# Optimization experiments

Measured on AMD Instinct MI355X. Metric: run time of the kernel, lower is better.

## Reference

```python
import jax, jax.numpy as jnp
import numpy as np

D_MODEL, D_STATE, D_CONV = 1024, 16, 4
BATCH, SEQ = 4, 2048
LN_EPS = 1e-5


def setup_inputs() -> dict:
    key = jax.random.key(0)
    ks = jax.random.split(key, 16)
    s_in = 1.0 / np.sqrt(D_MODEL)
    inp = {
        "x": jax.random.normal(ks[0], (BATCH, SEQ, D_MODEL), dtype=jnp.float32),
        "W_in": jax.random.normal(ks[1], (D_MODEL, 2 * D_MODEL), dtype=jnp.float32) * s_in,
        "b_in": jnp.zeros((2 * D_MODEL,), jnp.float32),
        "conv_w": jax.random.normal(ks[2], (D_MODEL, 1, D_CONV), dtype=jnp.float32) * 0.5,
        "conv_b": jnp.zeros((D_MODEL,), jnp.float32),
        "W_bc": jax.random.normal(ks[3], (D_MODEL, 2 * D_STATE), dtype=jnp.float32) * s_in,
        "b_bc": jnp.zeros((2 * D_STATE,), jnp.float32),
        "W_dt": jax.random.normal(ks[4], (D_MODEL, D_MODEL), dtype=jnp.float32) * s_in,
        "b_dt": jnp.zeros((D_MODEL,), jnp.float32),
        "A_log": jax.random.normal(ks[5], (D_MODEL, D_STATE), dtype=jnp.float32),
        "D": jnp.ones((D_MODEL,), jnp.float32),
        "W_out": jax.random.normal(ks[6], (D_MODEL, D_MODEL), dtype=jnp.float32) * s_in,
        "b_out": jnp.zeros((D_MODEL,), jnp.float32),
        "ln_g": jnp.ones((D_MODEL,), jnp.float32),
        "ln_b": jnp.zeros((D_MODEL,), jnp.float32),
    }
    return inp


def _causal_depthwise_conv(x_btd, conv_w, conv_b):
    # x_btd: (B, T, D). torch Conv1d(groups=D, padding=d_conv-1)[:, :, :T] == causal left-pad conv
    x_bdt = jnp.transpose(x_btd, (0, 2, 1))  # NCH
    y = jax.lax.conv_general_dilated(
        x_bdt, conv_w,
        window_strides=(1,), padding=[(D_CONV - 1, 0)],
        dimension_numbers=("NCH", "OIH", "NCH"),
        feature_group_count=D_MODEL)
    y = y + conv_b[None, :, None]
    return jnp.transpose(y, (0, 2, 1))


def _mamba_forward(x, W_in, b_in, conv_w, conv_b, W_bc, b_bc, W_dt, b_dt,
                   A_log, D, W_out, b_out, ln_g, ln_b):
    B_, T, _ = x.shape
    proj = x @ W_in + b_in                       # (B, T, 2D)
    x_ssm, x_gate = jnp.split(proj, 2, axis=-1)
    x_conv = jax.nn.silu(_causal_depthwise_conv(x_ssm, conv_w, conv_b))  # (B,T,D)
    BC = x_conv @ W_bc + b_bc                    # (B,T,2N)
    Bm, Cm = jnp.split(BC, 2, axis=-1)           # each (B,T,N)
    dt = jax.nn.softplus(x_conv @ W_dt + b_dt)   # (B,T,D)
    A = -jnp.exp(A_log)                          # (D,N)

    def step(h, inp):
        xt, dtt, Bt, Ct = inp                    # (B,D),(B,D),(B,N),(B,N)
        dA = jnp.exp(dtt[:, :, None] * A)        # (B,D,N)
        h = h * dA + (dtt * xt)[:, :, None] * Bt[:, None, :]
        y = jnp.einsum('bdn,bn->bd', h, Ct) + xt * D
        return h, y

    h0 = jnp.zeros((B_, D_MODEL, D_STATE), x.dtype)
    xs = (jnp.swapaxes(x_conv, 0, 1), jnp.swapaxes(dt, 0, 1),
          jnp.swapaxes(Bm, 0, 1), jnp.swapaxes(Cm, 0, 1))
    _, ys = jax.lax.scan(step, h0, xs)           # (T,B,D)
    y = jnp.swapaxes(ys, 0, 1)

    y = y * jax.nn.silu(x_gate)
    out = y @ W_out + b_out
    res = out + x
    mu = jnp.mean(res, axis=-1, keepdims=True)
    var = jnp.var(res, axis=-1, keepdims=True)
    return (res - mu) * jax.lax.rsqrt(var + LN_EPS) * ln_g + ln_b


def reference(x, W_in, b_in, conv_w, conv_b, W_bc, b_bc, W_dt, b_dt,
              A_log, D, W_out, b_out, ln_g, ln_b):
    return _mamba_forward(x, W_in, b_in, conv_w, conv_b, W_bc, b_bc,
                          W_dt, b_dt, A_log, D, W_out, b_out, ln_g, ln_b)
```

## Files before the change

kernel.cpp:

```cpp
#include <hip/hip_runtime.h>
#include <stdint.h>

#define D_MODEL 1024
#define T_SEQ   2048
#define N_BATCH 4
#define M_ROWS  (N_BATCH*T_SEQ)
#define N_STATE 16
#define SEGS    32
#define SEGLEN  (T_SEQ/SEGS)
#define CHUNK   8
#define NCHUNK  (SEGLEN/CHUNK)

typedef float  f32x4  __attribute__((ext_vector_type(4)));
typedef __bf16 bf16x8 __attribute__((ext_vector_type(8)));
typedef __bf16 bf16x4 __attribute__((ext_vector_type(4)));

__device__ __forceinline__ void gload16(const void* g, void* l) {
  __builtin_amdgcn_global_load_lds(
      (const __attribute__((address_space(1))) uint32_t*)g,
      (__attribute__((address_space(3))) uint32_t*)l, 16, 0, 0);
}

__device__ __forceinline__ float sigmoidf_(float v){ return 1.f/(1.f+__expf(-v)); }

__global__ __launch_bounds__(256) void cast_bf16_kernel(const float* __restrict__ in,
                                                        __bf16* __restrict__ out, int n4){
  int i = blockIdx.x*256 + threadIdx.x;
  if (i >= n4) return;
  float4 v = ((const float4*)in)[i];
  bf16x4 o; o[0]=(__bf16)v.x; o[1]=(__bf16)v.y; o[2]=(__bf16)v.z; o[3]=(__bf16)v.w;
  ((bf16x4*)out)[i] = o;
}

__global__ __launch_bounds__(256) void transpose_cast_kernel(const float* __restrict__ W,
                                                             __bf16* __restrict__ out,
                                                             int K, int N){
  __shared__ float tile[32][33];
  const int tx = threadIdx.x, ty = threadIdx.y;
  const int n0 = blockIdx.x*32, k0 = blockIdx.y*32;
  #pragma unroll
  for (int i=0;i<4;i++)
    tile[ty+i*8][tx] = W[(size_t)(k0+ty+i*8)*N + n0+tx];
  __syncthreads();
  #pragma unroll
  for (int i=0;i<4;i++)
    out[(size_t)(n0+ty+i*8)*K + k0+tx] = (__bf16)tile[tx][ty+i*8];
}

#define BK 32

template<int EPI, int BM, int BN, int NT>
__global__ __launch_bounds__(NT)
void gemm_bt(const __bf16* __restrict__ A, const __bf16* __restrict__ Bt,
             int N, int K,
             const float* __restrict__ bias0, const float* __restrict__ bias1,
             float* __restrict__ out0, float* __restrict__ out1,
             const float* __restrict__ addx,
             __bf16* __restrict__ out0b, __bf16* __restrict__ out1b)
{
  constexpr int NWAVE = NT/64;
  constexpr int WC_N  = NWAVE/2;
  constexpr int WM    = BM/2;
  constexpr int WN    = BN/WC_N;
  constexpr int MR    = WM/16, NR = WN/16;

  __shared__ __align__(16) __bf16 As[2][BM*BK];
  __shared__ __align__(16) __bf16 Bs[2][BN*BK];
  const int tid = threadIdx.x, wave = tid>>6, lane = tid&63;

  const int orig = blockIdx.y * gridDim.x + blockIdx.x;
  const int nwg  = gridDim.x * gridDim.y;
  const int cpx  = nwg >> 3;
  const int swz  = (orig & 7) * cpx + (orig >> 3);
  const int m0 = (swz / gridDim.x) * BM;
  const int n0 = (swz % gridDim.x) * BN;
  const int wr = wave / WC_N, wc = wave % WC_N;

  f32x4 acc[MR][NR];
  #pragma unroll
  for (int a=0;a<MR;a++)
    #pragma unroll
    for (int b=0;b<NR;b++) acc[a][b] = (f32x4){0.f,0.f,0.f,0.f};

  const int c0 = tid, c1 = tid + NT;
  const int r0 = c0>>2, s0 = (c0&3)*8;
  const int r1 = c1>>2, s1 = (c1&3)*8;
  const int arow = wr*WM + (lane&15), brow = wc*WN + (lane&15);
  const int kg = (lane>>4)*8;

  gload16(&A [(size_t)(m0+r0)*K + s0], &As[0][c0*8]);
  gload16(&A [(size_t)(m0+r1)*K + s1], &As[0][c1*8]);
  gload16(&Bt[(size_t)(n0+r0)*K + s0], &Bs[0][c0*8]);
  gload16(&Bt[(size_t)(n0+r1)*K + s1], &Bs[0][c1*8]);
  __syncthreads();

  const int nIter = K/BK;
  int buf = 0;
  for (int it=0; it<nIter; ++it){
    if (it+1 < nIter){
      const int kn = (it+1)*BK;
      gload16(&A [(size_t)(m0+r0)*K + kn + s0], &As[buf^1][c0*8]);
      gload16(&A [(size_t)(m0+r1)*K + kn + s1], &As[buf^1][c1*8]);
      gload16(&Bt[(size_t)(n0+r0)*K + kn + s0], &Bs[buf^1][c0*8]);
      gload16(&Bt[(size_t)(n0+r1)*K + kn + s1], &Bs[buf^1][c1*8]);
    }
    bf16x8 af[MR], bfv[NR];
    #pragma unroll
    for (int m=0;m<MR;m++) af[m]  = *(const bf16x8*)&As[buf][(arow+m*16)*BK + kg];
    #pragma unroll
    for (int n=0;n<NR;n++) bfv[n] = *(const bf16x8*)&Bs[buf][(brow+n*16)*BK + kg];
    #pragma unroll
    for (int m=0;m<MR;m++)
      #pragma unroll
      for (int n=0;n<NR;n++)
        acc[m][n] = __builtin_amdgcn_mfma_f32_16x16x32_bf16(af[m], bfv[n], acc[m][n], 0,0,0);
    __syncthreads();
    buf ^= 1;
  }

  const int cr = (lane>>4)*4, cc = lane&15;
  #pragma unroll
  for (int m=0;m<MR;m++){
    const int row = m0 + wr*WM + m*16 + cr;
    #pragma unroll
    for (int n=0;n<NR;n++){
      const int col = n0 + wc*WN + n*16 + cc;
      if (col >= N) continue;
      #pragma unroll
      for (int r=0;r<4;r++){
        float v = acc[m][n][r];
        const size_t ri = (size_t)(row + r);
        if constexpr (EPI==0){
          v += bias0[col];
          if (col < D_MODEL) out0b[ri*D_MODEL + col] = (__bf16)v;
          else               out1b[ri*D_MODEL + (col-D_MODEL)] = (__bf16)(v * sigmoidf_(v));
        } else if constexpr (EPI==1){
          if (col < D_MODEL){
            v += bias0[col];
            const float sp = (v > 20.f) ? v : __logf(1.f + __expf(v));
            out0b[ri*D_MODEL + col] = (__bf16)sp;
          } else {
            v += bias1[col-D_MODEL];
            out1[ri*32 + (col-D_MODEL)] = v;
          }
        } else {
          v += bias0[col] + addx[ri*D_MODEL + col];
          out0[ri*D_MODEL + col] = v;
        }
      }
    }
  }
}

__global__ __launch_bounds__(256) void conv_silu_kernel(
    const __bf16* __restrict__ xssm, const float* __restrict__ cw, const float* __restrict__ cb,
    __bf16* __restrict__ xcb)
{
  const int bt = blockIdx.x;
  const int t  = bt & (T_SEQ-1);
  const int d  = threadIdx.x*4;
  float4 w[4];
  #pragma unroll
  for (int j=0;j<4;j++) w[j] = *(const float4*)&cw[(d+j)*4];
  float4 acc = *(const float4*)&cb[d];
  #pragma unroll
  for (int k=0;k<4;k++){
    const int tt = t-3+k;
    if (tt >= 0){
      bf16x4 xv = ((const bf16x4*)xssm)[((size_t)(bt-3+k)*D_MODEL + d)>>2];
      acc.x = fmaf((float)xv[0], ((const float*)&w[0])[k], acc.x);
      acc.y = fmaf((float)xv[1], ((const float*)&w[1])[k], acc.y);
      acc.z = fmaf((float)xv[2], ((const float*)&w[2])[k], acc.z);
      acc.w = fmaf((float)xv[3], ((const float*)&w[3])[k], acc.w);
    }
  }
  acc.x *= sigmoidf_(acc.x); acc.y *= sigmoidf_(acc.y);
  acc.z *= sigmoidf_(acc.z); acc.w *= sigmoidf_(acc.w);
  bf16x4 o; o[0]=(__bf16)acc.x; o[1]=(__bf16)acc.y; o[2]=(__bf16)acc.z; o[3]=(__bf16)acc.w;
  ((bf16x4*)xcb)[((size_t)bt*D_MODEL + d)>>2] = o;
}

__global__ __launch_bounds__(128) void scan_p1(
    const __bf16* __restrict__ xcb, const __bf16* __restrict__ dtb, const float* __restrict__ BCb,
    const float* __restrict__ A_log, float* __restrict__ Ebuf, float* __restrict__ Pbuf)
{
  const int tid = threadIdx.x;
  const int d = blockIdx.x*128 + tid;
  const int b = blockIdx.y, sg = blockIdx.z;
  float an[16];
  {
    f32x4 a0 = *(const f32x4*)&A_log[(size_t)d*16];
    f32x4 a1 = *(const f32x4*)&A_log[(size_t)d*16+4];
    f32x4 a2 = *(const f32x4*)&A_log[(size_t)d*16+8];
    f32x4 a3 = *(const f32x4*)&A_log[(size_t)d*16+12];
    #pragma unroll
    for (int n=0;n<4;n++){ an[n]=-__expf(a0[n]); an[4+n]=-__expf(a1[n]);
                           an[8+n]=-__expf(a2[n]); an[12+n]=-__expf(a3[n]); }
  }
  __shared__ float sB[2][CHUNK][16];
  const size_t base = (size_t)b*T_SEQ + (size_t)sg*SEGLEN;
  const int sr = tid>>4, sc = tid&15;

  float dtr[CHUNK], xcr[CHUNK];
  sB[0][sr][sc] = BCb[(base + sr)*32 + sc];
  #pragma unroll
  for (int t=0;t<CHUNK;t++){
    dtr[t] = (float)dtb[(base+t)*D_MODEL + d];
    xcr[t] = (float)xcb[(base+t)*D_MODEL + d];
  }
  __syncthreads();

  float h[16];
  #pragma unroll
  for (int n=0;n<16;n++) h[n]=0.f;
  float sdt = 0.f;

  for (int c=0;c<NCHUNK;c++){
    float dtn[CHUNK], xcn[CHUNK], bnv = 0.f;
    if (c+1 < NCHUNK){
      const size_t nb = base + (size_t)(c+1)*CHUNK;
      #pragma unroll
      for (int t=0;t<CHUNK;t++){
        dtn[t] = (float)dtb[(nb+t)*D_MODEL + d];
        xcn[t] = (float)xcb[(nb+t)*D_MODEL + d];
      }
      bnv = BCb[(nb + sr)*32 + sc];
    }
    const int cb = c&1;
    #pragma unroll
    for (int t=0;t<CHUNK;t++){
      const float dtv = dtr[t], u = dtv*xcr[t];
      sdt += dtv;
      #pragma unroll
      for (int n=0;n<16;n++){
        const float dA = __expf(dtv*an[n]);
        h[n] = fmaf(h[n], dA, u*sB[cb][t][n]);
      }
    }
    if (c+1 < NCHUNK){
      sB[cb^1][sr][sc] = bnv;
      #pragma unroll
      for (int t=0;t<CHUNK;t++){ dtr[t]=dtn[t]; xcr[t]=xcn[t]; }
    }
    __syncthreads();
  }
  const size_t o = ((((size_t)sg*N_BATCH)+b)*D_MODEL + d)*16;
  #pragma unroll
  for (int n=0;n<16;n++){
    Ebuf[o+n] = h[n];
    Pbuf[o+n] = __expf(an[n]*sdt);
  }
}

__global__ __launch_bounds__(256) void scan_p2(float* __restrict__ Ebuf,
                                               const float* __restrict__ Pbuf)
{
  const size_t g = (size_t)blockIdx.x*256 + threadIdx.x;
  float c = 0.f;
  #pragma unroll
  for (int s=0;s<SEGS;s++){
    const size_t idx = (size_t)s*(N_BATCH*D_MODEL*N_STATE) + g;
    const float e = Ebuf[idx];
    const float p = Pbuf[idx];
    Ebuf[idx] = c;
    c = fmaf(p, c, e);
  }
}

__global__ __launch_bounds__(128) void scan_p3(
    const __bf16* __restrict__ xcb, const __bf16* __restrict__ dtb, const float* __restrict__ BCb,
    const float* __restrict__ A_log, const float* __restrict__ Dvec,
    const __bf16* __restrict__ gsil, const float* __restrict__ Ebuf,
    __bf16* __restrict__ ybf)
{
  const int tid = threadIdx.x;
  const int d = blockIdx.x*128 + tid;
  const int b = blockIdx.y, sg = blockIdx.z;
  float an[16];
  {
    f32x4 a0 = *(const f32x4*)&A_log[(size_t)d*16];
    f32x4 a1 = *(const f32x4*)&A_log[(size_t)d*16+4];
    f32x4 a2 = *(const f32x4*)&A_log[(size_t)d*16+8];
    f32x4 a3 = *(const f32x4*)&A_log[(size_t)d*16+12];
    #pragma unroll
    for (int n=0;n<4;n++){ an[n]=-__expf(a0[n]); an[4+n]=-__expf(a1[n]);
                           an[8+n]=-__expf(a2[n]); an[12+n]=-__expf(a3[n]); }
  }
  const float Dd = Dvec[d];
  __shared__ float sBC[2][CHUNK][32];
  const size_t base = (size_t)b*T_SEQ + (size_t)sg*SEGLEN;
  const int sr = tid>>4, sc = tid&15;

  float h[16];
  {
    const size_t o = ((((size_t)sg*N_BATCH)+b)*D_MODEL + d)*16;
    f32x4 e0 = *(const f32x4*)&Ebuf[o];
    f32x4 e1 = *(const f32x4*)&Ebuf[o+4];
    f32x4 e2 = *(const f32x4*)&Ebuf[o+8];
    f32x4 e3 = *(const f32x4*)&Ebuf[o+12];
    #pragma unroll
    for (int n=0;n<4;n++){ h[n]=e0[n]; h[4+n]=e1[n]; h[8+n]=e2[n]; h[12+n]=e3[n]; }
  }

  float dtr[CHUNK], xcr[CHUNK], gsr[CHUNK];
  sBC[0][sr][sc]    = BCb[(base + sr)*32 + sc];
  sBC[0][sr][16+sc] = BCb[(base + sr)*32 + 16 + sc];
  #pragma unroll
  for (int t=0;t<CHUNK;t++){
    dtr[t] = (float)dtb[(base+t)*D_MODEL + d];
    xcr[t] = (float)xcb[(base+t)*D_MODEL + d];
    gsr[t] = (float)gsil[(base+t)*D_MODEL + d];
  }
  __syncthreads();

  for (int c=0;c<NCHUNK;c++){
    float dtn[CHUNK], xcn[CHUNK], gsn[CHUNK], bnv=0.f, cnv=0.f;
    if (c+1 < NCHUNK){
      const size_t nb = base + (size_t)(c+1)*CHUNK;
      #pragma unroll
      for (int t=0;t<CHUNK;t++){
        dtn[t] = (float)dtb[(nb+t)*D_MODEL + d];
        xcn[t] = (float)xcb[(nb+t)*D_MODEL + d];
        gsn[t] = (float)gsil[(nb+t)*D_MODEL + d];
      }
      bnv = BCb[(nb + sr)*32 + sc];
      cnv = BCb[(nb + sr)*32 + 16 + sc];
    }
    const int cb = c&1;
    #pragma unroll
    for (int t=0;t<CHUNK;t++){
      const float dtv = dtr[t], xcv = xcr[t], u = dtv*xcv;
      #pragma unroll
      for (int n=0;n<16;n++){
        const float dA = __expf(dtv*an[n]);
        h[n] = fmaf(h[n], dA, u*sBC[cb][t][n]);
      }
      float yv = Dd*xcv;
      #pragma unroll
      for (int n=0;n<16;n++) yv = fmaf(h[n], sBC[cb][t][16+n], yv);
      ybf[(base + (size_t)c*CHUNK + t)*D_MODEL + d] = (__bf16)(yv * gsr[t]);
    }
    if (c+1 < NCHUNK){
      sBC[cb^1][sr][sc]    = bnv;
      sBC[cb^1][sr][16+sc] = cnv;
      #pragma unroll
      for (int t=0;t<CHUNK;t++){ dtr[t]=dtn[t]; xcr[t]=xcn[t]; gsr[t]=gsn[t]; }
    }
    __syncthreads();
  }
}

__global__ __launch_bounds__(256) void ln_kernel(float* __restrict__ io,
    const float* __restrict__ g, const float* __restrict__ b)
{
  const int row = blockIdx.x, tid = threadIdx.x;
  float4* p = (float4*)(io + (size_t)row*D_MODEL);
  float4 v = p[tid];
  float s  = v.x+v.y+v.z+v.w;
  float s2 = v.x*v.x + v.y*v.y + v.z*v.z + v.w*v.w;
  #pragma unroll
  for (int o=1;o<64;o<<=1){ s += __shfl_xor(s,o); s2 += __shfl_xor(s2,o); }
  __shared__ float red[8];
  const int wave = tid>>6, lane = tid&63;
  if (lane==0){ red[wave]=s; red[4+wave]=s2; }
  __syncthreads();
  s  = red[0]+red[1]+red[2]+red[3];
  s2 = red[4]+red[5]+red[6]+red[7];
  const float mu  = s*(1.f/D_MODEL);
  const float var = s2*(1.f/D_MODEL) - mu*mu;
  const float rs  = rsqrtf(var + 1e-5f);
  float4 gg = ((const float4*)g)[tid], bb = ((const float4*)b)[tid];
  float4 o;
  o.x = (v.x-mu)*rs*gg.x + bb.x;
  o.y = (v.y-mu)*rs*gg.y + bb.y;
  o.z = (v.z-mu)*rs*gg.z + bb.z;
  o.w = (v.w-mu)*rs*gg.w + bb.w;
  p[tid] = o;
}

extern "C" void kernel_launch(void* const* d_in, const int* in_sizes, int n_in,
                              void* d_out, int out_size, void* d_ws, size_t ws_size,
                              hipStream_t stream)
{
  (void)in_sizes; (void)n_in; (void)out_size; (void)ws_size;
  const float* x      = (const float*)d_in[0];
  const float* W_in   = (const float*)d_in[1];
  const float* b_in   = (const float*)d_in[2];
  const float* conv_w = (const float*)d_in[3];
  const float* conv_b = (const float*)d_in[4];
  const float* W_bc   = (const float*)d_in[5];
  const float* b_bc   = (const float*)d_in[6];
  const float* W_dt   = (const float*)d_in[7];
  const float* b_dt   = (const float*)d_in[8];
  const float* A_log  = (const float*)d_in[9];
  const float* Dv     = (const float*)d_in[10];
  const float* W_out  = (const float*)d_in[11];
  const float* b_out  = (const float*)d_in[12];
  const float* ln_g   = (const float*)d_in[13];
  const float* ln_b   = (const float*)d_in[14];

  char* Wp = (char*)d_ws;
  __bf16* x_bf    = (__bf16*)(Wp + 0);
  __bf16* WinT    = (__bf16*)(Wp + 16777216);
  __bf16* WdbT    = (__bf16*)(Wp + 20971520);
  __bf16* WoutT   = (__bf16*)(Wp + 23592960);
  __bf16* xssm_bf = (__bf16*)(Wp + 25690112);
  float*  Ebuf    = (float*) (Wp + 42467328);
  float*  Pbuf    = (float*) (Wp + 50855936);
  __bf16* gsil_bf = (__bf16*)(Wp + 59244544);
  __bf16* xcb     = (__bf16*)(Wp + 76021760);
  __bf16* dtb     = (__bf16*)(Wp + 92798976);
  float*  BCb     = (float*) (Wp + 109576192);
  __bf16* ybf     = (__bf16*)(Wp + 110624768);

  hipMemsetAsync(WdbT, 0, (size_t)1280*1024*2, stream);

  cast_bf16_kernel<<<8192,256,0,stream>>>(x, x_bf, (M_ROWS*D_MODEL)/4);
  transpose_cast_kernel<<<dim3(64,32), dim3(32,8),0,stream>>>(W_in,  WinT,  1024, 2048);
  transpose_cast_kernel<<<dim3(32,32), dim3(32,8),0,stream>>>(W_dt,  WdbT,  1024, 1024);
  transpose_cast_kernel<<<dim3(1,32),  dim3(32,8),0,stream>>>(W_bc,  WdbT + (size_t)1024*1024, 1024, 32);
  transpose_cast_kernel<<<dim3(32,32), dim3(32,8),0,stream>>>(W_out, WoutT, 1024, 1024);

  gemm_bt<0,256,256,512><<<dim3(8,32),512,0,stream>>>(x_bf, WinT, 2048, 1024, b_in, nullptr,
                                           nullptr, nullptr, nullptr, xssm_bf, gsil_bf);
  conv_silu_kernel<<<M_ROWS,256,0,stream>>>(xssm_bf, conv_w, conv_b, xcb);
  gemm_bt<1,256,256,512><<<dim3(5,32),512,0,stream>>>(xcb, WdbT, 1056, 1024, b_dt, b_bc,
                                          nullptr, BCb, nullptr, dtb, nullptr);

  scan_p1<<<dim3(8,4,SEGS),128,0,stream>>>(xcb, dtb, BCb, A_log, Ebuf, Pbuf);
  scan_p2<<<256,256,0,stream>>>(Ebuf, Pbuf);
  scan_p3<<<dim3(8,4,SEGS),128,0,stream>>>(xcb, dtb, BCb, A_log, Dv, gsil_bf, Ebuf, ybf);

  gemm_bt<2,128,128,256><<<dim3(8,64),256,0,stream>>>(ybf, WoutT, 1024, 1024, b_out, nullptr,
                                          (float*)d_out, nullptr, x, nullptr, nullptr);
  ln_kernel<<<M_ROWS,256,0,stream>>>((float*)d_out, ln_g, ln_b);
}
```

Before: 420.1 us.

## Fuse prep kernels, shrink GEMM tiles, and double scan segments

Merges the x cast, the four weight transpose-casts and the padding memset into a single prep_kernel launch, which cuts launch overhead. The in-projection and dt/BC GEMMs switch from 256x256 tiles with 512 threads to 128x128 tiles with 256 threads, so they launch more blocks and fill more CUs. The scan now uses 64 segments instead of 32 for more parallelism, and the workspace layout is reshuffled to make room for the larger E/P buffers. The risks are less data reuse per GEMM tile and a longer sequential combine pass over the segments.

```diff
diff --git a/kernel.cpp b/kernel.cpp
--- a/kernel.cpp
+++ b/kernel.cpp
@@ -6,7 +6,7 @@
 #define N_BATCH 4
 #define M_ROWS  (N_BATCH*T_SEQ)
 #define N_STATE 16
-#define SEGS    32
+#define SEGS    64
 #define SEGLEN  (T_SEQ/SEGS)
 #define CHUNK   8
 #define NCHUNK  (SEGLEN/CHUNK)
@@ -23,21 +23,38 @@
 
 __device__ __forceinline__ float sigmoidf_(float v){ return 1.f/(1.f+__expf(-v)); }
 
-__global__ __launch_bounds__(256) void cast_bf16_kernel(const float* __restrict__ in,
-                                                        __bf16* __restrict__ out, int n4){
-  int i = blockIdx.x*256 + threadIdx.x;
-  if (i >= n4) return;
-  float4 v = ((const float4*)in)[i];
-  bf16x4 o; o[0]=(__bf16)v.x; o[1]=(__bf16)v.y; o[2]=(__bf16)v.z; o[3]=(__bf16)v.w;
-  ((bf16x4*)out)[i] = o;
-}
-
-__global__ __launch_bounds__(256) void transpose_cast_kernel(const float* __restrict__ W,
-                                                             __bf16* __restrict__ out,
-                                                             int K, int N){
+__global__ __launch_bounds__(256) void prep_kernel(
+    const float* __restrict__ x, __bf16* __restrict__ x_bf,
+    const float* __restrict__ W_in, __bf16* __restrict__ WinT,
+    const float* __restrict__ W_dt, const float* __restrict__ W_bc, __bf16* __restrict__ WdbT,
+    const float* __restrict__ W_out, __bf16* __restrict__ WoutT)
+{
   __shared__ float tile[32][33];
-  const int tx = threadIdx.x, ty = threadIdx.y;
-  const int n0 = blockIdx.x*32, k0 = blockIdx.y*32;
+  const int bid = blockIdx.x, tid = threadIdx.x;
+
+  if (bid < 8192){
+    const int i = bid*256 + tid;
+    float4 v = ((const float4*)x)[i];
+    bf16x4 o; o[0]=(__bf16)v.x; o[1]=(__bf16)v.y; o[2]=(__bf16)v.z; o[3]=(__bf16)v.w;
+    ((bf16x4*)x_bf)[i] = o;
+    return;
+  }
+  int b2 = bid - 8192;
+  const float* W; __bf16* out; int K, N, xt, yt;
+  if (b2 < 2048){ W=W_in; out=WinT; K=1024; N=2048; xt=b2&63; yt=b2>>6; }
+  else if ((b2 -= 2048) < 1024){ W=W_dt; out=WdbT; K=1024; N=1024; xt=b2&31; yt=b2>>5; }
+  else if ((b2 -= 1024) < 32){ W=W_bc; out=WdbT+(size_t)1024*1024; K=1024; N=32; xt=0; yt=b2; }
+  else if ((b2 -= 32) < 1024){ W=W_out; out=WoutT; K=1024; N=1024; xt=b2&31; yt=b2>>5; }
+  else {
+    b2 -= 1024;
+    bf16x8 z;
+    #pragma unroll
+    for (int i=0;i<8;i++) z[i] = (__bf16)0.f;
+    *(bf16x8*)&WdbT[(size_t)1056*1024 + (size_t)b2*2048 + tid*8] = z;
+    return;
+  }
+  const int tx = tid&31, ty = tid>>5;
+  const int n0 = xt*32, k0 = yt*32;
   #pragma unroll
   for (int i=0;i<4;i++)
     tile[ty+i*8][tx] = W[(size_t)(k0+ty+i*8)*N + n0+tx];
@@ -403,28 +420,22 @@
   __bf16* x_bf    = (__bf16*)(Wp + 0);
   __bf16* WinT    = (__bf16*)(Wp + 16777216);
   __bf16* WdbT    = (__bf16*)(Wp + 20971520);
-  __bf16* WoutT   = (__bf16*)(Wp + 23592960);
-  __bf16* xssm_bf = (__bf16*)(Wp + 25690112);
-  float*  Ebuf    = (float*) (Wp + 42467328);
-  float*  Pbuf    = (float*) (Wp + 50855936);
-  __bf16* gsil_bf = (__bf16*)(Wp + 59244544);
-  __bf16* xcb     = (__bf16*)(Wp + 76021760);
-  __bf16* dtb     = (__bf16*)(Wp + 92798976);
-  float*  BCb     = (float*) (Wp + 109576192);
-  __bf16* ybf     = (__bf16*)(Wp + 110624768);
-
-  hipMemsetAsync(WdbT, 0, (size_t)1280*1024*2, stream);
-
-  cast_bf16_kernel<<<8192,256,0,stream>>>(x, x_bf, (M_ROWS*D_MODEL)/4);
-  transpose_cast_kernel<<<dim3(64,32), dim3(32,8),0,stream>>>(W_in,  WinT,  1024, 2048);
-  transpose_cast_kernel<<<dim3(32,32), dim3(32,8),0,stream>>>(W_dt,  WdbT,  1024, 1024);
-  transpose_cast_kernel<<<dim3(1,32),  dim3(32,8),0,stream>>>(W_bc,  WdbT + (size_t)1024*1024, 1024, 32);
-  transpose_cast_kernel<<<dim3(32,32), dim3(32,8),0,stream>>>(W_out, WoutT, 1024, 1024);
-
-  gemm_bt<0,256,256,512><<<dim3(8,32),512,0,stream>>>(x_bf, WinT, 2048, 1024, b_in, nullptr,
+  __bf16* WoutT   = (__bf16*)(Wp + 23330816);
+  __bf16* xssm_bf = (__bf16*)(Wp + 25427968);
+  __bf16* gsil_bf = (__bf16*)(Wp + 42205184);
+  __bf16* xcb     = (__bf16*)(Wp + 58982400);
+  __bf16* dtb     = (__bf16*)(Wp + 75759616);
+  float*  BCb     = (float*) (Wp + 92536832);
+  __bf16* ybf     = (__bf16*)(Wp + 93585408);
+  float*  Ebuf    = (float*) (Wp + 110362624);
+  float*  Pbuf    = (float*) (Wp + 127139840);
+
+  prep_kernel<<<12368,256,0,stream>>>(x, x_bf, W_in, WinT, W_dt, W_bc, WdbT, W_out, WoutT);
+
+  gemm_bt<0,128,128,256><<<dim3(16,64),256,0,stream>>>(x_bf, WinT, 2048, 1024, b_in, nullptr,
                                            nullptr, nullptr, nullptr, xssm_bf, gsil_bf);
   conv_silu_kernel<<<M_ROWS,256,0,stream>>>(xssm_bf, conv_w, conv_b, xcb);
-  gemm_bt<1,256,256,512><<<dim3(5,32),512,0,stream>>>(xcb, WdbT, 1056, 1024, b_dt, b_bc,
+  gemm_bt<1,128,128,256><<<dim3(9,64),256,0,stream>>>(xcb, WdbT, 1056, 1024, b_dt, b_bc,
                                           nullptr, BCb, nullptr, dtb, nullptr);
 
   scan_p1<<<dim3(8,4,SEGS),128,0,stream>>>(xcb, dtb, BCb, A_log, Ebuf, Pbuf);
```

After: 389.9 us. -7.2%, faster.
